# Optimization experiments

Hardware: AMD Instinct MI355X
Metric: run time of the kernel (lower is better)

The kernel has to match this reference:

```python
import jax, jax.numpy as jnp
import numpy as np


def setup_inputs() -> dict:
    key = jax.random.key(0)
    k1, k2, k3, k4, k5 = jax.random.split(key, 5)
    n_mol, n_atm, d_feat, n_props = 128, 64, 384, 64
    n_ref = n_mol * n_atm  # 8192 reference atoms (flattened)
    # element labels in {1,2,3,4} (e.g. H,C,N,O); all atoms nondummy (Z>0)
    Z_ref = jax.random.randint(k1, (n_mol, n_atm), 1, 5)
    Z = jax.random.randint(k2, (n_mol, n_atm), 1, 5)
    # descriptors, scaled so the poly kernel K^expK stays O(1)
    scale = 1.0 / np.sqrt(d_feat).astype(np.float32)
    X_ref = jax.random.normal(k3, (n_ref, d_feat), jnp.float32) * scale
    desc = jax.random.normal(k4, (n_mol, n_atm, d_feat), jnp.float32) * scale
    Alpha = jax.random.normal(k5, (n_props, n_ref), jnp.float32)
    return {"Alpha": Alpha, "X_ref": X_ref, "desc": desc,
            "Z_ref": Z_ref, "Z": Z, "expK": 2}


def reference(Alpha, X_ref, desc, Z_ref, Z, expK):
    # Faithful dense formulation of the per-element gather/matmul/scatter:
    # y[p, j] = sum_i Alpha[p, i] * (X_ref[i] . X_in[j])^expK * [Z_ref[i] == Z[j]]
    # Each query atom j belongs to exactly one element, so the masked dense
    # kernel reproduces the grouped computation exactly (same flat ordering
    # as torch's molecule-major concatenation).
    d_feat = X_ref.shape[-1]
    X_in = desc.reshape(-1, d_feat)                      # [N_in, d]
    K = jnp.power(X_ref @ X_in.T, expK)                  # [N_ref, N_in]
    mask = Z_ref.reshape(-1)[:, None] == Z.reshape(-1)[None, :]
    y = Alpha @ jnp.where(mask, K, jnp.float32(0.0))     # [n_props, N_in]
    return y
```

## Files before the change

kernel.cpp:

```cpp
#include <hip/hip_runtime.h>
#include <hip/hip_bf16.h>
#include <stdint.h>


typedef __attribute__((ext_vector_type(8))) short bf16x8;
typedef __attribute__((ext_vector_type(4))) float f32x4;
typedef __attribute__((ext_vector_type(4))) unsigned int u32x4;

#define DFEAT  384
#define NREF   8192
#define NIN    8192
#define NPROPS 64
#define BJ 128
#define BI 128
#define BK 32
#define KSTEPS (DFEAT / BK)
#define CAP    8704
#define NSTRIP (CAP / BJ)

__device__ __forceinline__ void gload_lds16(const void* g, void* l) {
  __builtin_amdgcn_global_load_lds(
      (const __attribute__((address_space(1))) void*)g,
      (__attribute__((address_space(3))) void*)l,
      16, 0, 0);
}

__device__ __forceinline__ unsigned short bfbits(float f) {
  __hip_bfloat16 h = __float2bfloat16(f);
  return __builtin_bit_cast(unsigned short, h);
}

__device__ __forceinline__ float pwr(float s, int expK) {
  if (expK == 2) return s * s;
  float r = 1.0f;
  for (int e = 0; e < expK; ++e) r *= s;
  return r;
}

__global__ __launch_bounds__(256) void partition2_kernel(
    const int* __restrict__ Za, const int* __restrict__ Zb,
    int* __restrict__ perma, int* __restrict__ permb,
    int* __restrict__ goffa, int* __restrict__ goffb) {
  const int* Zin = blockIdx.x ? Zb : Za;
  int* perm = blockIdx.x ? permb : perma;
  int* goff = blockIdx.x ? goffb : goffa;

  __shared__ int cnt[256][4];
  __shared__ int gstart[4];
  __shared__ int gtot[4];
  const int t = threadIdx.x;
  const int base = t * 32;

  int c[4] = {0, 0, 0, 0};
  int zloc[32];
  #pragma unroll
  for (int e = 0; e < 32; ++e) {
    zloc[e] = (Zin[base + e] - 1) & 3;
    ++c[zloc[e]];
  }
  #pragma unroll
  for (int b = 0; b < 4; ++b) cnt[t][b] = c[b];
  __syncthreads();

  const int w = t >> 6, l = t & 63;
  {
    int v0 = cnt[4 * l + 0][w], v1 = cnt[4 * l + 1][w];
    int v2 = cnt[4 * l + 2][w], v3 = cnt[4 * l + 3][w];
    int s = v0 + v1 + v2 + v3;
    int inc = s;
    #pragma unroll
    for (int d = 1; d < 64; d <<= 1) {
      int o = __shfl_up(inc, d, 64);
      if (l >= d) inc += o;
    }
    const int excl = inc - s;
    cnt[4 * l + 0][w] = excl;
    cnt[4 * l + 1][w] = excl + v0;
    cnt[4 * l + 2][w] = excl + v0 + v1;
    cnt[4 * l + 3][w] = excl + v0 + v1 + v2;
    if (l == 63) gtot[w] = inc;
  }
  __syncthreads();

  if (t == 0) {
    int off = 0;
    #pragma unroll
    for (int b = 0; b < 4; ++b) {
      gstart[b] = off; goff[b] = off;
      off += ((gtot[b] + 127) >> 7) << 7;
    }
    goff[4] = off;
  }
  __syncthreads();

  for (int s = t; s < CAP; s += 256) perm[s] = -1;
  __syncthreads();

  int pos[4];
  #pragma unroll
  for (int b = 0; b < 4; ++b) pos[b] = gstart[b] + cnt[t][b];
  #pragma unroll
  for (int e = 0; e < 32; ++e) {
    const int z = zloc[e];
    perm[pos[z]++] = base + e;
  }
}

#define XSEC (CAP * (DFEAT / 4) / 256)
__global__ void gather_all(const float* __restrict__ Xr_in,
                           const float* __restrict__ Xi_in,
                           const float* __restrict__ Al_in,
                           const int* __restrict__ perm_i,
                           const int* __restrict__ perm_j,
                           __hip_bfloat16* __restrict__ Xr_g,
                           __hip_bfloat16* __restrict__ Xi_g,
                           __hip_bfloat16* __restrict__ Ab_g) {
  const int b = blockIdx.x;
  if (b < 2 * XSEC) {
    const bool isA = (b < XSEC);
    const float* in = isA ? Xr_in : Xi_in;
    const int* perm = isA ? perm_i : perm_j;
    __hip_bfloat16* out = isA ? Xr_g : Xi_g;
    const int idx = (isA ? b : b - XSEC) * 256 + threadIdx.x;
    const int per_row = DFEAT / 4;
    const int slot = idx / per_row;
    const int c4 = (idx % per_row) * 4;
    const int src = perm[slot];
    ushort4 o = make_ushort4(0, 0, 0, 0);
    if (src >= 0) {
      float4 v = *reinterpret_cast<const float4*>(in + (size_t)src * DFEAT + c4);
      o.x = bfbits(v.x); o.y = bfbits(v.y); o.z = bfbits(v.z); o.w = bfbits(v.w);
    }
    *reinterpret_cast<ushort4*>(out + (size_t)slot * DFEAT + c4) = o;
  } else {
    const int t = (b - 2 * XSEC) * 256 + threadIdx.x;
    const int per_row = CAP / 4;
    const int p  = t / per_row;
    const int c4 = t % per_row;
    const int blk = c4 >> 3;
    const int g   = c4 & 7;
    const int l4g = g >> 1;
    const int eh  = g & 1;
    ushort4 o;
    unsigned short* op = &o.x;
    #pragma unroll
    for (int r = 0; r < 4; ++r) {
      const int slot = blk * 32 + eh * 16 + l4g * 4 + r;
      const int src = perm_i[slot];
      op[r] = (src >= 0) ? bfbits(Al_in[(size_t)p * NREF + src]) : (unsigned short)0;
    }
    *reinterpret_cast<ushort4*>(Ab_g + (size_t)p * CAP + blk * 32 + l4g * 8 + eh * 4) = o;
  }
}

__global__ void reduce_scatter(const float* __restrict__ partial,
                               const int* __restrict__ permj,
                               float* __restrict__ out, int nsplit) {
  const int idx = blockIdx.x * blockDim.x + threadIdx.x;
  const int per_row = CAP / 4;
  const int p = idx / per_row;
  const int s4 = (idx % per_row) * 4;
  float4 s = make_float4(0.f, 0.f, 0.f, 0.f);
  for (int sp = 0; sp < nsplit; ++sp) {
    float4 v = *reinterpret_cast<const float4*>(
        partial + (size_t)sp * NPROPS * CAP + (size_t)p * CAP + s4);
    s.x += v.x; s.y += v.y; s.z += v.z; s.w += v.w;
  }
  const int4 dst = *reinterpret_cast<const int4*>(permj + s4);
  float* po = out + (size_t)p * NIN;
  if (dst.x >= 0) po[dst.x] = s.x;
  if (dst.y >= 0) po[dst.y] = s.y;
  if (dst.z >= 0) po[dst.z] = s.z;
  if (dst.w >= 0) po[dst.w] = s.w;
}

__global__ __launch_bounds__(512, 4) void fused_poly_kernel(
    const __hip_bfloat16* __restrict__ Xr,
    const __hip_bfloat16* __restrict__ Xi,
    const __hip_bfloat16* __restrict__ Abp,
    const int* __restrict__ ioff,
    const int* __restrict__ joff,
    const int* __restrict__ expKp,
    float* __restrict__ partial,
    int nsplit, int chunk)
{
  const int flat = blockIdx.x;
  const int newflat = (flat & 7) * chunk + (flat >> 3);
  const int strip = newflat / nsplit;
  const int split = newflat % nsplit;
  const int j0 = strip * BJ;
  if (j0 >= joff[4]) return;

  int grp = 0;
  grp += (j0 >= joff[1]);
  grp += (j0 >= joff[2]);
  grp += (j0 >= joff[3]);
  const int ibase = ioff[grp];
  const int ntiles_g = (ioff[grp + 1] - ibase) / BI;
  const int tb = ntiles_g / nsplit;
  const int rem = ntiles_g % nsplit;
  const int ntiles = tb + (split < rem ? 1 : 0);
  const int tile_begin = split * tb + (split < rem ? split : rem);

  const int tid  = threadIdx.x;
  const int wid  = tid >> 6;
  const int lane = tid & 63;
  const int l15  = lane & 15;
  const int l4   = lane >> 4;
  const int wi   = wid >> 2;
  const int wj   = wid & 3;

  __shared__ char smem[32768];
  __hip_bfloat16* lA = (__hip_bfloat16*)smem;
  __hip_bfloat16* lB = (__hip_bfloat16*)(smem + 16384);

  const int expK = *expKp;

  const int srow = lane >> 2;
  const int scol = ((lane & 3) ^ (srow & 3)) * 8;

  auto stage = [&](int buf, int i0s, int kks) {
    const int grow = wid * 16 + srow;
    const size_t gc = (size_t)kks * BK + scol;
    gload_lds16(Xr + (size_t)(i0s + grow) * DFEAT + gc, lA + buf * 4096 + wid * 512);
    gload_lds16(Xi + (size_t)(j0  + grow) * DFEAT + gc, lB + buf * 4096 + wid * 512);
  };

  f32x4 accO[4][2];
  #pragma unroll
  for (int a = 0; a < 4; ++a)
    #pragma unroll
    for (int n = 0; n < 2; ++n)
      accO[a][n] = (f32x4){0.f, 0.f, 0.f, 0.f};

  if (ntiles > 0) {
    int cur = 0;
    stage(0, ibase + tile_begin * BI, 0);
    asm volatile("s_waitcnt vmcnt(0)" ::: "memory");
    __builtin_amdgcn_s_barrier();

    for (int t = 0; t < ntiles; ++t) {
      const int i0 = ibase + (tile_begin + t) * BI;

      f32x4 acc[4][2];
      #pragma unroll
      for (int m = 0; m < 4; ++m)
        #pragma unroll
        for (int n = 0; n < 2; ++n)
          acc[m][n] = (f32x4){0.f, 0.f, 0.f, 0.f};

      for (int kk = 0; kk < KSTEPS; ++kk) {
        if (kk < KSTEPS - 1) {
          stage(cur ^ 1, i0, kk + 1);
        } else if (t < ntiles - 1) {
          stage(cur ^ 1, i0 + BI, 0);
        }

        __builtin_amdgcn_s_setprio(1);
        {
          bf16x8 aF[4], bF[2];
          #pragma unroll
          for (int m = 0; m < 4; ++m) {
            const int rA = wi * 64 + m * 16 + l15;
            aF[m] = *reinterpret_cast<const bf16x8*>(
                (char*)(lA + cur * 4096) + rA * 64 + ((l4 ^ (rA & 3)) << 4));
          }
          #pragma unroll
          for (int n = 0; n < 2; ++n) {
            const int rB = wj * 32 + n * 16 + l15;
            bF[n] = *reinterpret_cast<const bf16x8*>(
                (char*)(lB + cur * 4096) + rB * 64 + ((l4 ^ (rB & 3)) << 4));
          }
          #pragma unroll
          for (int m = 0; m < 4; ++m)
            #pragma unroll
            for (int n = 0; n < 2; ++n)
              acc[m][n] = __builtin_amdgcn_mfma_f32_16x16x32_bf16(
                  aF[m], bF[n], acc[m][n], 0, 0, 0);
        }
        __builtin_amdgcn_s_setprio(0);
        asm volatile("s_waitcnt vmcnt(0) lgkmcnt(0)" ::: "memory");
        __builtin_amdgcn_s_barrier();
        cur ^= 1;
      }

      #pragma unroll
      for (int ks = 0; ks < 2; ++ks) {
        bf16x8 aP[4];
        #pragma unroll
        for (int a = 0; a < 4; ++a)
          aP[a] = *reinterpret_cast<const bf16x8*>(
              Abp + (size_t)(a * 16 + l15) * CAP + i0 + wi * 64 + ks * 32 + l4 * 8);
        #pragma unroll
        for (int n = 0; n < 2; ++n) {
          const f32x4 s0 = acc[2 * ks][n];
          const f32x4 s1 = acc[2 * ks + 1][n];
          u32x4 tw;
          tw[0] = (uint32_t)bfbits(pwr(s0[0], expK)) |
                  ((uint32_t)bfbits(pwr(s0[1], expK)) << 16);
          tw[1] = (uint32_t)bfbits(pwr(s0[2], expK)) |
                  ((uint32_t)bfbits(pwr(s0[3], expK)) << 16);
          tw[2] = (uint32_t)bfbits(pwr(s1[0], expK)) |
                  ((uint32_t)bfbits(pwr(s1[1], expK)) << 16);
          tw[3] = (uint32_t)bfbits(pwr(s1[2], expK)) |
                  ((uint32_t)bfbits(pwr(s1[3], expK)) << 16);
          const bf16x8 bP = __builtin_bit_cast(bf16x8, tw);
          __builtin_amdgcn_s_setprio(1);
          #pragma unroll
          for (int a = 0; a < 4; ++a)
            accO[a][n] = __builtin_amdgcn_mfma_f32_16x16x32_bf16(
                aP[a], bP, accO[a][n], 0, 0, 0);
          __builtin_amdgcn_s_setprio(0);
        }
      }
    }
  }

  __syncthreads();
  float* rb = (float*)smem;
  if (wi == 1) {
    #pragma unroll
    for (int a = 0; a < 4; ++a)
      #pragma unroll
      for (int n = 0; n < 2; ++n)
        #pragma unroll
        for (int r = 0; r < 4; ++r)
          rb[wj * 2048 + (a * 16 + l4 * 4 + r) * 32 + n * 16 + l15] =
              accO[a][n][r];
  }
  __syncthreads();
  if (wi == 0) {
    float* po = partial + (size_t)split * NPROPS * CAP;
    #pragma unroll
    for (int a = 0; a < 4; ++a)
      #pragma unroll
      for (int n = 0; n < 2; ++n)
        #pragma unroll
        for (int r = 0; r < 4; ++r) {
          const int p = a * 16 + l4 * 4 + r;
          const int jl = wj * 32 + n * 16 + l15;
          po[(size_t)p * CAP + j0 + jl] =
              accO[a][n][r] + rb[wj * 2048 + p * 32 + n * 16 + l15];
        }
  }
}

extern "C" void kernel_launch(void* const* d_in, const int* in_sizes, int n_in,
                              void* d_out, int out_size, void* d_ws, size_t ws_size,
                              hipStream_t stream) {
  (void)in_sizes; (void)n_in; (void)out_size;
  const float* Alpha = (const float*)d_in[0];
  const float* X_ref = (const float*)d_in[1];
  const float* desc  = (const float*)d_in[2];
  const int*   Z_ref = (const int*)d_in[3];
  const int*   Z     = (const int*)d_in[4];
  const int*   expK  = (const int*)d_in[5];
  float* out = (float*)d_out;

  char* ws = (char*)d_ws;
  size_t off = 0;
  auto alloc = [&](size_t b) { void* p = ws + off; off = (off + b + 255) & ~255ULL; return p; };

  int* perm_i = (int*)alloc(CAP * 4);
  int* perm_j = (int*)alloc(CAP * 4);
  int* ioff   = (int*)alloc(8 * 4);
  int* joff   = (int*)alloc(8 * 4);
  __hip_bfloat16* Xr_g = (__hip_bfloat16*)alloc((size_t)CAP * DFEAT * 2);
  __hip_bfloat16* Xi_g = (__hip_bfloat16*)alloc((size_t)CAP * DFEAT * 2);
  __hip_bfloat16* Ab_g = (__hip_bfloat16*)alloc((size_t)NPROPS * CAP * 2);

  int nsplit = 8;
  while (nsplit > 1 && off + (size_t)nsplit * NPROPS * CAP * 4 > ws_size) nsplit >>= 1;
  float* partial = (float*)alloc((size_t)nsplit * NPROPS * CAP * 4);

  partition2_kernel<<<dim3(2), 256, 0, stream>>>(
      Z_ref, Z, perm_i, perm_j, ioff, joff);

  gather_all<<<dim3(2 * XSEC + NPROPS * (CAP / 4) / 256), 256, 0, stream>>>(
      X_ref, desc, Alpha, perm_i, perm_j, Xr_g, Xi_g, Ab_g);

  const int grid = NSTRIP * nsplit;
  fused_poly_kernel<<<dim3(grid), 512, 0, stream>>>(
      Xr_g, Xi_g, Ab_g, ioff, joff, expK, partial, nsplit, grid / 8);

  reduce_scatter<<<dim3(NPROPS * (CAP / 4) / 256), 256, 0, stream>>>(
      partial, perm_j, out, nsplit);
}
```

Measured before the change: 76.73 us.

## Use 4-wave blocks with larger per-wave tiles and triple-buffered LDS pipeline

The fused kernel moves from 8 waves to 4 waves per block, with each wave computing a 64x64 output sub-tile instead of 64x32. This raises MFMA work per LDS fragment load. Staging becomes a three-stage LDS ring prefetching two K-steps ahead with partial vmcnt waits, replacing the full drain at every step, and uses a new swizzle. The split factor rises from 8 to 12, giving more blocks, at the cost of more register pressure and a larger partial-sum buffer to reduce.

```diff
diff --git a/kernel.cpp b/kernel.cpp
--- a/kernel.cpp
+++ b/kernel.cpp
@@ -174,7 +174,7 @@
   if (dst.w >= 0) po[dst.w] = s.w;
 }
 
-__global__ __launch_bounds__(512, 4) void fused_poly_kernel(
+__global__ __launch_bounds__(256, 3) void fused_poly_kernel(
     const __hip_bfloat16* __restrict__ Xr,
     const __hip_bfloat16* __restrict__ Xi,
     const __hip_bfloat16* __restrict__ Abp,
@@ -207,81 +207,95 @@
   const int lane = tid & 63;
   const int l15  = lane & 15;
   const int l4   = lane >> 4;
-  const int wi   = wid >> 2;
-  const int wj   = wid & 3;
-
-  __shared__ char smem[32768];
-  __hip_bfloat16* lA = (__hip_bfloat16*)smem;
-  __hip_bfloat16* lB = (__hip_bfloat16*)(smem + 16384);
+  const int wi   = wid >> 1;
+  const int wj   = wid & 1;
+
+  __shared__ char smem[49152];
 
   const int expK = *expKp;
 
+  const int rsl = (l4 ^ ((l15 >> 1) & 3)) << 4;
+  const int scol = ((lane & 3) ^ ((lane >> 3) & 3)) * 8;
   const int srow = lane >> 2;
-  const int scol = ((lane & 3) ^ (srow & 3)) * 8;
 
   auto stage = [&](int buf, int i0s, int kks) {
-    const int grow = wid * 16 + srow;
-    const size_t gc = (size_t)kks * BK + scol;
-    gload_lds16(Xr + (size_t)(i0s + grow) * DFEAT + gc, lA + buf * 4096 + wid * 512);
-    gload_lds16(Xi + (size_t)(j0  + grow) * DFEAT + gc, lB + buf * 4096 + wid * 512);
+    char* Ab_ = smem + buf * 16384;
+    char* Bb_ = smem + buf * 16384 + 8192;
+    #pragma unroll
+    for (int q = 0; q < 2; ++q) {
+      const int grow = wid * 32 + q * 16 + srow;
+      const size_t gc = (size_t)kks * BK + scol;
+      gload_lds16(Xr + (size_t)(i0s + grow) * DFEAT + gc,
+                  Ab_ + wid * 2048 + q * 1024);
+      gload_lds16(Xi + (size_t)(j0 + grow) * DFEAT + gc,
+                  Bb_ + wid * 2048 + q * 1024);
+    }
   };
 
-  f32x4 accO[4][2];
+  f32x4 accO[4][4];
   #pragma unroll
   for (int a = 0; a < 4; ++a)
     #pragma unroll
-    for (int n = 0; n < 2; ++n)
+    for (int n = 0; n < 4; ++n)
       accO[a][n] = (f32x4){0.f, 0.f, 0.f, 0.f};
 
   if (ntiles > 0) {
-    int cur = 0;
     stage(0, ibase + tile_begin * BI, 0);
-    asm volatile("s_waitcnt vmcnt(0)" ::: "memory");
-    __builtin_amdgcn_s_barrier();
+    stage(1, ibase + tile_begin * BI, 1);
 
     for (int t = 0; t < ntiles; ++t) {
-      const int i0 = ibase + (tile_begin + t) * BI;
-
-      f32x4 acc[4][2];
+      const int i0c = ibase + (tile_begin + t) * BI;
+      const int i0n = i0c + BI;
+
+      f32x4 acc[4][4];
       #pragma unroll
       for (int m = 0; m < 4; ++m)
         #pragma unroll
-        for (int n = 0; n < 2; ++n)
+        for (int n = 0; n < 4; ++n)
           acc[m][n] = (f32x4){0.f, 0.f, 0.f, 0.f};
 
-      for (int kk = 0; kk < KSTEPS; ++kk) {
-        if (kk < KSTEPS - 1) {
-          stage(cur ^ 1, i0, kk + 1);
-        } else if (t < ntiles - 1) {
-          stage(cur ^ 1, i0 + BI, 0);
+      #pragma unroll
+      for (int ph = 0; ph < KSTEPS; ++ph) {
+        const int cb = ph % 3;
+        const int sb = (ph + 2) % 3;
+        if (ph <= 9) {
+          stage(sb, i0c, ph + 2);
+          asm volatile("s_waitcnt vmcnt(8)" ::: "memory");
+        } else if (t + 1 < ntiles) {
+          stage(sb, i0n, ph - 10);
+          asm volatile("s_waitcnt vmcnt(8)" ::: "memory");
+        } else if (ph == 10) {
+          asm volatile("s_waitcnt vmcnt(4)" ::: "memory");
+        } else {
+          asm volatile("s_waitcnt vmcnt(0)" ::: "memory");
         }
-
+        __builtin_amdgcn_s_barrier();
+
+        char* Ab_ = smem + cb * 16384;
+        char* Bb_ = smem + cb * 16384 + 8192;
         __builtin_amdgcn_s_setprio(1);
         {
-          bf16x8 aF[4], bF[2];
+          bf16x8 aF[4], bF[4];
           #pragma unroll
           for (int m = 0; m < 4; ++m) {
             const int rA = wi * 64 + m * 16 + l15;
-            aF[m] = *reinterpret_cast<const bf16x8*>(
-                (char*)(lA + cur * 4096) + rA * 64 + ((l4 ^ (rA & 3)) << 4));
+            aF[m] = *reinterpret_cast<const bf16x8*>(Ab_ + rA * 64 + rsl);
           }
           #pragma unroll
-          for (int n = 0; n < 2; ++n) {
-            const int rB = wj * 32 + n * 16 + l15;
-            bF[n] = *reinterpret_cast<const bf16x8*>(
-                (char*)(lB + cur * 4096) + rB * 64 + ((l4 ^ (rB & 3)) << 4));
+          for (int n = 0; n < 4; ++n) {
+            const int rB = wj * 64 + n * 16 + l15;
+            bF[n] = *reinterpret_cast<const bf16x8*>(Bb_ + rB * 64 + rsl);
           }
           #pragma unroll
           for (int m = 0; m < 4; ++m)
             #pragma unroll
-            for (int n = 0; n < 2; ++n)
+            for (int n = 0; n < 4; ++n)
               acc[m][n] = __builtin_amdgcn_mfma_f32_16x16x32_bf16(
                   aF[m], bF[n], acc[m][n], 0, 0, 0);
         }
         __builtin_amdgcn_s_setprio(0);
-        asm volatile("s_waitcnt vmcnt(0) lgkmcnt(0)" ::: "memory");
+        asm volatile("s_waitcnt lgkmcnt(0)" ::: "memory");
         __builtin_amdgcn_s_barrier();
-        cur ^= 1;
       }
 
       #pragma unroll
@@ -290,9 +304,9 @@
         #pragma unroll
         for (int a = 0; a < 4; ++a)
           aP[a] = *reinterpret_cast<const bf16x8*>(
-              Abp + (size_t)(a * 16 + l15) * CAP + i0 + wi * 64 + ks * 32 + l4 * 8);
+              Abp + (size_t)(a * 16 + l15) * CAP + i0c + wi * 64 + ks * 32 + l4 * 8);
         #pragma unroll
-        for (int n = 0; n < 2; ++n) {
+        for (int n = 0; n < 4; ++n) {
           const f32x4 s0 = acc[2 * ks][n];
           const f32x4 s1 = acc[2 * ks + 1][n];
           u32x4 tw;
@@ -322,10 +336,10 @@
     #pragma unroll
     for (int a = 0; a < 4; ++a)
       #pragma unroll
-      for (int n = 0; n < 2; ++n)
+      for (int n = 0; n < 4; ++n)
         #pragma unroll
         for (int r = 0; r < 4; ++r)
-          rb[wj * 2048 + (a * 16 + l4 * 4 + r) * 32 + n * 16 + l15] =
+          rb[wj * 4096 + (a * 16 + l4 * 4 + r) * 64 + n * 16 + l15] =
               accO[a][n][r];
   }
   __syncthreads();
@@ -334,13 +348,13 @@
     #pragma unroll
     for (int a = 0; a < 4; ++a)
       #pragma unroll
-      for (int n = 0; n < 2; ++n)
+      for (int n = 0; n < 4; ++n)
         #pragma unroll
         for (int r = 0; r < 4; ++r) {
           const int p = a * 16 + l4 * 4 + r;
-          const int jl = wj * 32 + n * 16 + l15;
+          const int jl = wj * 64 + n * 16 + l15;
           po[(size_t)p * CAP + j0 + jl] =
-              accO[a][n][r] + rb[wj * 2048 + p * 32 + n * 16 + l15];
+              accO[a][n][r] + rb[wj * 4096 + p * 64 + n * 16 + l15];
         }
   }
 }
@@ -369,8 +383,8 @@
   __hip_bfloat16* Xi_g = (__hip_bfloat16*)alloc((size_t)CAP * DFEAT * 2);
   __hip_bfloat16* Ab_g = (__hip_bfloat16*)alloc((size_t)NPROPS * CAP * 2);
 
-  int nsplit = 8;
-  while (nsplit > 1 && off + (size_t)nsplit * NPROPS * CAP * 4 > ws_size) nsplit >>= 1;
+  int nsplit = 12;
+  while (nsplit > 4 && off + (size_t)nsplit * NPROPS * CAP * 4 > ws_size) nsplit -= 4;
   float* partial = (float*)alloc((size_t)nsplit * NPROPS * CAP * 4);
 
   partition2_kernel<<<dim3(2), 256, 0, stream>>>(
@@ -380,7 +394,7 @@
       X_ref, desc, Alpha, perm_i, perm_j, Xr_g, Xi_g, Ab_g);
 
   const int grid = NSTRIP * nsplit;
-  fused_poly_kernel<<<dim3(grid), 512, 0, stream>>>(
+  fused_poly_kernel<<<dim3(grid), 256, 0, stream>>>(
       Xr_g, Xi_g, Ab_g, ioff, joff, expK, partial, nsplit, grid / 8);
 
   reduce_scatter<<<dim3(NPROPS * (CAP / 4) / 256), 256, 0, stream>>>(
```

New measurement: 99.33 us. 29.5% more time.
